# Optimization experiments

Hardware: AMD Instinct MI355X
Metric: run time of the kernel (lower is better)

Reference implementation:

```python
import jax, jax.numpy as jnp
import numpy as np

B, D, DP, H = 65536, 512, 256, 8
HD = D // H  # head dim = 64
EPS = 1e-5


def _layernorm(x, gamma, beta):
    mu = jnp.mean(x, axis=-1, keepdims=True)
    var = jnp.var(x, axis=-1, keepdims=True)
    return (x - mu) * jax.lax.rsqrt(var + EPS) * gamma + beta


def setup_inputs() -> dict:
    key = jax.random.key(0)
    ks = jax.random.split(key, 16)
    n = lambda k, shape, s=0.02: (jax.random.normal(k, shape, jnp.float32) * s)
    return {
        "cell_emb": jax.random.normal(ks[0], (B, D), jnp.float32),
        "pert_emb": jax.random.normal(ks[1], (B, DP), jnp.float32),
        # perturbation_proj: Linear(DP -> D)
        "Wp": n(ks[2], (D, DP)), "bp": jnp.zeros((D,), jnp.float32),
        # MultiheadAttention in/out projections (each D x D)
        "Wq": n(ks[3], (D, D)), "bq": jnp.zeros((D,), jnp.float32),
        "Wk": n(ks[4], (D, D)), "bk": jnp.zeros((D,), jnp.float32),
        "Wv": n(ks[5], (D, D)), "bv": jnp.zeros((D,), jnp.float32),
        "Wo": n(ks[6], (D, D)), "bo": jnp.zeros((D,), jnp.float32),
        # norm1, norm2
        "g1": jnp.ones((D,), jnp.float32), "be1": jnp.zeros((D,), jnp.float32),
        "g2": jnp.ones((D,), jnp.float32), "be2": jnp.zeros((D,), jnp.float32),
        # FFN: Linear(D -> 2D), GELU, Linear(2D -> D)
        "W1": n(ks[7], (2 * D, D)), "b1": jnp.zeros((2 * D,), jnp.float32),
        "W2": n(ks[8], (D, 2 * D)), "b2": jnp.zeros((D,), jnp.float32),
    }


def reference(cell_emb, pert_emb, Wp, bp, Wq, bq, Wk, bk, Wv, bv, Wo, bo,
              g1, be1, g2, be2, W1, b1, W2, b2):
    # kv = perturbation_proj(pert_emb), length-1 KV sequence
    kv = pert_emb @ Wp.T + bp                       # (B, D)
    # MultiheadAttention with q_len = kv_len = 1
    q = (cell_emb @ Wq.T + bq).reshape(B, H, HD)    # (B, H, HD)
    k = (kv @ Wk.T + bk).reshape(B, H, HD)
    v = (kv @ Wv.T + bv).reshape(B, H, HD)
    # scores over a single key -> softmax yields 1, kept for faithfulness
    logits = jnp.sum(q * k, axis=-1, keepdims=True) / jnp.sqrt(jnp.float32(HD))  # (B, H, 1)
    w = jax.nn.softmax(logits, axis=-1)             # == ones (single key)
    attn = (w * v).reshape(B, D)
    attn_out = attn @ Wo.T + bo                     # (B, D)
    x = _layernorm(cell_emb + attn_out, g1, be1)
    # FFN with exact (erf) GELU, matching torch nn.GELU default
    h = jax.nn.gelu(x @ W1.T + b1, approximate=False)
    ffn_out = h @ W2.T + b2
    return _layernorm(x + ffn_out, g2, be2)
```

## Files before the change

kernel.cpp:

```cpp
#include <hip/hip_runtime.h>
#include <hip/hip_bf16.h>

typedef __bf16 bf16_t;
typedef __attribute__((ext_vector_type(8))) __bf16 bf16x8;
typedef __attribute__((ext_vector_type(4))) float f32x4;

__global__ void prep_wvp(const float* __restrict__ Wv, const float* __restrict__ Wp,
                         const float* __restrict__ bp, const float* __restrict__ bv,
                         float* __restrict__ Wvp, float* __restrict__ bvp) {
  const int i = blockIdx.x;
  const int j = threadIdx.x;
  float a = 0.f;
  for (int d = 0; d < 512; ++d) a += Wv[i * 512 + d] * Wp[d * 256 + j];
  Wvp[i * 256 + j] = a;
  if (j == 0) {
    float b = 0.f;
    for (int d = 0; d < 512; ++d) b += Wv[i * 512 + d] * bp[d];
    bvp[i] = b + bv[i];
  }
}

__global__ void prep_wc(const float* __restrict__ Wo, const float* __restrict__ bo,
                        const float* __restrict__ Wvp, const float* __restrict__ bvp,
                        bf16_t* __restrict__ Wc, float* __restrict__ bcomb) {
  const int o = blockIdx.x;
  const int j = threadIdx.x;
  float a = 0.f;
  for (int i = 0; i < 512; ++i) a += Wo[o * 512 + i] * Wvp[i * 256 + j];
  const int g = o >> 4, rr = o & 15, t = j >> 5, q = (j >> 3) & 3, e = j & 7;
  Wc[((((size_t)g * 8 + t) * 64) + q * 16 + rr) * 8 + e] = (bf16_t)a;
  if (j == 0) {
    float b = 0.f;
    for (int i = 0; i < 512; ++i) b += Wo[o * 512 + i] * bvp[i];
    bcomb[o] = b + bo[o];
  }
}

__global__ void prep_cast(const float* __restrict__ W1, const float* __restrict__ W2,
                          bf16_t* __restrict__ W1b, bf16_t* __restrict__ W2b) {
  const int idx = (blockIdx.x * 256 + threadIdx.x) * 8;
  const float* s;
  bf16_t* d;
  if (idx < 524288) {
    const int o = idx >> 9, k = idx & 511;
    const int g = o >> 4, rr = o & 15, t = k >> 5, q = (k >> 3) & 3;
    s = W1 + idx;
    d = W1b + ((((size_t)g * 16 + t) * 64) + q * 16 + rr) * 8;
  } else {
    const int i2 = idx - 524288;
    const int o = i2 >> 10, k = i2 & 1023;
    const int g = o >> 4, rr = o & 15, t = k >> 5, q = (k >> 3) & 3;
    s = W2 + i2;
    d = W2b + ((((size_t)g * 32 + t) * 64) + q * 16 + rr) * 8;
  }
  float4 u0 = *(const float4*)s;
  float4 u1 = *(const float4*)(s + 4);
  bf16x8 v;
  v[0] = (bf16_t)u0.x; v[1] = (bf16_t)u0.y; v[2] = (bf16_t)u0.z; v[3] = (bf16_t)u0.w;
  v[4] = (bf16_t)u1.x; v[5] = (bf16_t)u1.y; v[6] = (bf16_t)u1.z; v[7] = (bf16_t)u1.w;
  *(bf16x8*)d = v;
}


__device__ __forceinline__ int alay(int row, int k) {
  const int rr = row & 15;
  const int c = (k >> 3) & 3;
  return (((k >> 5) & 15) * 4 + (row >> 4)) * 512 +
         (rr * 4 + (c ^ ((rr >> 1) & 3))) * 8 + (k & 7);
}

template <int STEPS>
__device__ __forceinline__ void kloop8(const bf16_t* __restrict__ lA_,
                                       const bf16_t* __restrict__ Bp,
                                       int g0, int SB, int soff,
                                       int fRd, int awin, int lane,
                                       f32x4 (&acc)[2][8]) {
  auto bfrag = [&](int j, int s) {
    return *(const bf16x8*)(Bp + ((size_t)((g0 + j) * SB + (soff + s)) * 64 + lane) * 8);
  };
  bf16x8 bA[4], bB[4];
#pragma unroll
  for (int j = 0; j < 4; ++j) bA[j] = bfrag(j, 0);
#pragma unroll 2
  for (int s = 0; s < STEPS; ++s) {
#pragma unroll
    for (int j = 0; j < 4; ++j) bB[j] = bfrag(4 + j, s);
    bf16x8 af[2];
#pragma unroll
    for (int i = 0; i < 2; ++i)
      af[i] = *(const bf16x8*)&lA_[(s * 4 + awin + i) * 512 + fRd];
    __builtin_amdgcn_s_setprio(1);
#pragma unroll
    for (int j = 0; j < 4; ++j)
#pragma unroll
      for (int i = 0; i < 2; ++i)
        acc[i][j] = __builtin_amdgcn_mfma_f32_16x16x32_bf16(af[i], bA[j], acc[i][j], 0, 0, 0);
    __builtin_amdgcn_s_setprio(0);
    if (s + 1 < STEPS) {
#pragma unroll
      for (int j = 0; j < 4; ++j) bA[j] = bfrag(j, s + 1);
    }
    __builtin_amdgcn_s_setprio(1);
#pragma unroll
    for (int j = 0; j < 4; ++j)
#pragma unroll
      for (int i = 0; i < 2; ++i)
        acc[i][4 + j] = __builtin_amdgcn_mfma_f32_16x16x32_bf16(af[i], bB[j], acc[i][4 + j], 0, 0, 0);
    __builtin_amdgcn_s_setprio(0);
  }
}

__global__ __launch_bounds__(512, 1) void fused_block(
    const float* __restrict__ pert, const bf16_t* __restrict__ Wc,
    const float* __restrict__ bcomb, const float* __restrict__ cell,
    const float* __restrict__ g1, const float* __restrict__ be1,
    const bf16_t* __restrict__ W1b, const float* __restrict__ b1,
    const bf16_t* __restrict__ W2b, const float* __restrict__ b2,
    const float* __restrict__ g2, const float* __restrict__ be2,
    float* __restrict__ out) {

  __shared__ __align__(16) bf16_t lX[64 * 512];
  __shared__ __align__(16) bf16_t lH[64 * 512];
  __shared__ float rs[4][64];
  __shared__ float rss[4][64];

  const int t = threadIdx.x;
  const int m0 = blockIdx.x * 64;
  const int lane = t & 63;
  const int w = t >> 6;
  const int wr = w >> 2;
  const int wc = w & 3;
  const int r = lane & 15;
  const int q = lane >> 4;
  const int qs = q ^ ((r >> 1) & 3);
  const int fRd = r * 32 + qs * 8;
  const int awin = 2 * wr;

#pragma unroll
  for (int u = 0; u < 4; ++u) {
    const int g = u * 512 + t;
    const int row = g >> 5;
    const int c = g & 31;
    const float* src = pert + (size_t)(m0 + row) * 256 + c * 8;
    float4 u0 = *(const float4*)src;
    float4 u1 = *(const float4*)(src + 4);
    bf16x8 v;
    v[0] = (bf16_t)u0.x; v[1] = (bf16_t)u0.y; v[2] = (bf16_t)u0.z; v[3] = (bf16_t)u0.w;
    v[4] = (bf16_t)u1.x; v[5] = (bf16_t)u1.y; v[6] = (bf16_t)u1.z; v[7] = (bf16_t)u1.w;
    *(bf16x8*)&lH[alay(row, c * 8)] = v;
  }
  __syncthreads();

  f32x4 acc1[2][8];
#pragma unroll
  for (int i = 0; i < 2; ++i)
#pragma unroll
    for (int j = 0; j < 8; ++j)
#pragma unroll
      for (int p = 0; p < 4; ++p) acc1[i][j][p] = 0.f;

  kloop8<8>(lH, Wc, 8 * wc, 8, 0, fRd, awin, lane, acc1);

  {
    float s_[2][4], ss_[2][4];
#pragma unroll
    for (int i = 0; i < 2; ++i)
#pragma unroll
      for (int p = 0; p < 4; ++p) { s_[i][p] = 0.f; ss_[i][p] = 0.f; }
    float bb[8];
#pragma unroll
    for (int j = 0; j < 8; ++j) bb[j] = bcomb[128 * wc + 16 * j + r];
#pragma unroll
    for (int i = 0; i < 2; ++i)
#pragma unroll
      for (int p = 0; p < 4; ++p) {
        const int rowl = 32 * wr + 16 * i + 4 * q + p;
#pragma unroll
        for (int j = 0; j < 8; ++j) {
          const int col = 128 * wc + 16 * j + r;
          float v = acc1[i][j][p] + bb[j] + cell[(size_t)(m0 + rowl) * 512 + col];
          acc1[i][j][p] = v;
          s_[i][p] += v;
          ss_[i][p] += v * v;
        }
      }
#pragma unroll
    for (int m = 1; m <= 8; m <<= 1)
#pragma unroll
      for (int i = 0; i < 2; ++i)
#pragma unroll
        for (int p = 0; p < 4; ++p) {
          s_[i][p] += __shfl_xor(s_[i][p], m);
          ss_[i][p] += __shfl_xor(ss_[i][p], m);
        }
    if (r == 0) {
#pragma unroll
      for (int i = 0; i < 2; ++i)
#pragma unroll
        for (int p = 0; p < 4; ++p) {
          const int rowl = 32 * wr + 16 * i + 4 * q + p;
          rs[wc][rowl] = s_[i][p];
          rss[wc][rowl] = ss_[i][p];
        }
    }
    __syncthreads();
    float mu[2][4], inv[2][4];
#pragma unroll
    for (int i = 0; i < 2; ++i)
#pragma unroll
      for (int p = 0; p < 4; ++p) {
        const int rowl = 32 * wr + 16 * i + 4 * q + p;
        float tS = rs[0][rowl] + rs[1][rowl] + rs[2][rowl] + rs[3][rowl];
        float tQ = rss[0][rowl] + rss[1][rowl] + rss[2][rowl] + rss[3][rowl];
        float m_ = tS * (1.0f / 512.0f);
        float v_ = tQ * (1.0f / 512.0f) - m_ * m_;
        mu[i][p] = m_;
        inv[i][p] = rsqrtf(v_ + 1e-5f);
      }
    float ga[8], be[8];
#pragma unroll
    for (int j = 0; j < 8; ++j) {
      ga[j] = g1[128 * wc + 16 * j + r];
      be[j] = be1[128 * wc + 16 * j + r];
    }
#pragma unroll
    for (int i = 0; i < 2; ++i)
#pragma unroll
      for (int p = 0; p < 4; ++p) {
        const int rowl = 32 * wr + 16 * i + 4 * q + p;
#pragma unroll
        for (int j = 0; j < 8; ++j) {
          const int col = 128 * wc + 16 * j + r;
          float v = (acc1[i][j][p] - mu[i][p]) * inv[i][p] * ga[j] + be[j];
          lX[alay(rowl, col)] = (bf16_t)v;
        }
      }
  }
  __syncthreads();

  f32x4 acc3[2][8];
#pragma unroll
  for (int i = 0; i < 2; ++i)
#pragma unroll
    for (int j = 0; j < 8; ++j)
#pragma unroll
      for (int p = 0; p < 4; ++p) acc3[i][j][p] = 0.f;

  for (int hh = 0; hh < 2; ++hh) {
#pragma unroll
    for (int i = 0; i < 2; ++i)
#pragma unroll
      for (int j = 0; j < 8; ++j)
#pragma unroll
        for (int p = 0; p < 4; ++p) acc1[i][j][p] = 0.f;
    kloop8<16>(lX, W1b, 32 * hh + 8 * wc, 16, 0, fRd, awin, lane, acc1);
    {
      float bb1[8];
#pragma unroll
      for (int j = 0; j < 8; ++j) bb1[j] = b1[512 * hh + 128 * wc + 16 * j + r];
#pragma unroll
      for (int i = 0; i < 2; ++i)
#pragma unroll
        for (int p = 0; p < 4; ++p) {
          const int rowl = 32 * wr + 16 * i + 4 * q + p;
#pragma unroll
          for (int j = 0; j < 8; ++j) {
            const int col = 128 * wc + 16 * j + r;
            float v = acc1[i][j][p] + bb1[j];
            float g = 0.5f * v * (1.0f + erff(v * 0.70710678118654752f));
            lH[alay(rowl, col)] = (bf16_t)g;
          }
        }
    }
    __syncthreads();
    kloop8<16>(lH, W2b, 8 * wc, 32, 16 * hh, fRd, awin, lane, acc3);
    if (hh == 0) __syncthreads();
  }

  {
    float s_[2][4], ss_[2][4];
#pragma unroll
    for (int i = 0; i < 2; ++i)
#pragma unroll
      for (int p = 0; p < 4; ++p) { s_[i][p] = 0.f; ss_[i][p] = 0.f; }
    float bb2[8];
#pragma unroll
    for (int j = 0; j < 8; ++j) bb2[j] = b2[128 * wc + 16 * j + r];
#pragma unroll
    for (int i = 0; i < 2; ++i)
#pragma unroll
      for (int p = 0; p < 4; ++p) {
        const int rowl = 32 * wr + 16 * i + 4 * q + p;
#pragma unroll
        for (int j = 0; j < 8; ++j) {
          const int col = 128 * wc + 16 * j + r;
          float v = acc3[i][j][p] + bb2[j] + (float)lX[alay(rowl, col)];
          acc3[i][j][p] = v;
          s_[i][p] += v;
          ss_[i][p] += v * v;
        }
      }
#pragma unroll
    for (int m = 1; m <= 8; m <<= 1)
#pragma unroll
      for (int i = 0; i < 2; ++i)
#pragma unroll
        for (int p = 0; p < 4; ++p) {
          s_[i][p] += __shfl_xor(s_[i][p], m);
          ss_[i][p] += __shfl_xor(ss_[i][p], m);
        }
    __syncthreads();
    if (r == 0) {
#pragma unroll
      for (int i = 0; i < 2; ++i)
#pragma unroll
        for (int p = 0; p < 4; ++p) {
          const int rowl = 32 * wr + 16 * i + 4 * q + p;
          rs[wc][rowl] = s_[i][p];
          rss[wc][rowl] = ss_[i][p];
        }
    }
    __syncthreads();
    float mu[2][4], inv[2][4];
#pragma unroll
    for (int i = 0; i < 2; ++i)
#pragma unroll
      for (int p = 0; p < 4; ++p) {
        const int rowl = 32 * wr + 16 * i + 4 * q + p;
        float tS = rs[0][rowl] + rs[1][rowl] + rs[2][rowl] + rs[3][rowl];
        float tQ = rss[0][rowl] + rss[1][rowl] + rss[2][rowl] + rss[3][rowl];
        float m_ = tS * (1.0f / 512.0f);
        float v_ = tQ * (1.0f / 512.0f) - m_ * m_;
        mu[i][p] = m_;
        inv[i][p] = rsqrtf(v_ + 1e-5f);
      }
    float ga[8], be[8];
#pragma unroll
    for (int j = 0; j < 8; ++j) {
      ga[j] = g2[128 * wc + 16 * j + r];
      be[j] = be2[128 * wc + 16 * j + r];
    }
#pragma unroll
    for (int i = 0; i < 2; ++i)
#pragma unroll
      for (int p = 0; p < 4; ++p) {
        const int rowl = 32 * wr + 16 * i + 4 * q + p;
#pragma unroll
        for (int j = 0; j < 8; ++j) {
          const int col = 128 * wc + 16 * j + r;
          out[(size_t)(m0 + rowl) * 512 + col] =
              (acc3[i][j][p] - mu[i][p]) * inv[i][p] * ga[j] + be[j];
        }
      }
  }
}

extern "C" void kernel_launch(void* const* d_in, const int* in_sizes, int n_in,
                              void* d_out, int out_size, void* d_ws, size_t ws_size,
                              hipStream_t stream) {
  const float* cell = (const float*)d_in[0];
  const float* pert = (const float*)d_in[1];
  const float* Wp   = (const float*)d_in[2];
  const float* bp   = (const float*)d_in[3];
  const float* Wv   = (const float*)d_in[8];
  const float* bv   = (const float*)d_in[9];
  const float* Wo   = (const float*)d_in[10];
  const float* bo   = (const float*)d_in[11];
  const float* g1   = (const float*)d_in[12];
  const float* be1  = (const float*)d_in[13];
  const float* g2   = (const float*)d_in[14];
  const float* be2  = (const float*)d_in[15];
  const float* W1   = (const float*)d_in[16];
  const float* b1   = (const float*)d_in[17];
  const float* W2   = (const float*)d_in[18];
  const float* b2   = (const float*)d_in[19];

  char* ws = (char*)d_ws;
  float*  Wvp   = (float*)(ws + 0);
  float*  bvp   = (float*)(ws + 524288);
  float*  bcomb = (float*)(ws + 526336);
  bf16_t* Wc    = (bf16_t*)(ws + 528384);
  bf16_t* W1b   = (bf16_t*)(ws + 790528);
  bf16_t* W2b   = (bf16_t*)(ws + 1839104);
  (void)in_sizes; (void)n_in; (void)out_size; (void)ws_size;

  prep_wvp<<<512, 256, 0, stream>>>(Wv, Wp, bp, bv, Wvp, bvp);
  prep_wc<<<512, 256, 0, stream>>>(Wo, bo, Wvp, bvp, Wc, bcomb);
  prep_cast<<<512, 256, 0, stream>>>(W1, W2, W1b, W2b);

  fused_block<<<1024, 512, 0, stream>>>(pert, Wc, bcomb, cell, g1, be1,
                                        W1b, b1, W2b, b2, g2, be2,
                                        (float*)d_out);
}
```

Baseline: 651.9 us.

## Split FFN hidden dimension into four quarter chunks to shrink LDS and registers

The FFN hidden dimension is now processed in four 256-wide chunks instead of two 512-wide halves. The GELU intermediate buffer in LDS is halved and the per-chunk accumulator drops to 2x4 tiles, reducing register and shared-memory pressure. The kloop helper is generalized to take a template N-tile count. In exchange there are more barriers and more, shorter K-loops, with less B-fragment reuse per A load in the W1 stage.

```diff
diff --git a/kernel.cpp b/kernel.cpp
--- a/kernel.cpp
+++ b/kernel.cpp
@@ -69,43 +69,44 @@
          (rr * 4 + (c ^ ((rr >> 1) & 3))) * 8 + (k & 7);
 }
 
-template <int STEPS>
-__device__ __forceinline__ void kloop8(const bf16_t* __restrict__ lA_,
-                                       const bf16_t* __restrict__ Bp,
-                                       int g0, int SB, int soff,
-                                       int fRd, int awin, int lane,
-                                       f32x4 (&acc)[2][8]) {
+template <int STEPS, int NJ>
+__device__ __forceinline__ void kloop(const bf16_t* __restrict__ lA_,
+                                      const bf16_t* __restrict__ Bp,
+                                      int g0, int SB, int soff,
+                                      int fRd, int awin, int lane,
+                                      f32x4 (&acc)[2][NJ]) {
+  constexpr int H = NJ / 2;
   auto bfrag = [&](int j, int s) {
     return *(const bf16x8*)(Bp + ((size_t)((g0 + j) * SB + (soff + s)) * 64 + lane) * 8);
   };
-  bf16x8 bA[4], bB[4];
-#pragma unroll
-  for (int j = 0; j < 4; ++j) bA[j] = bfrag(j, 0);
+  bf16x8 bA[H], bB[H];
+#pragma unroll
+  for (int j = 0; j < H; ++j) bA[j] = bfrag(j, 0);
 #pragma unroll 2
   for (int s = 0; s < STEPS; ++s) {
 #pragma unroll
-    for (int j = 0; j < 4; ++j) bB[j] = bfrag(4 + j, s);
+    for (int j = 0; j < H; ++j) bB[j] = bfrag(H + j, s);
     bf16x8 af[2];
 #pragma unroll
     for (int i = 0; i < 2; ++i)
       af[i] = *(const bf16x8*)&lA_[(s * 4 + awin + i) * 512 + fRd];
     __builtin_amdgcn_s_setprio(1);
 #pragma unroll
-    for (int j = 0; j < 4; ++j)
+    for (int j = 0; j < H; ++j)
 #pragma unroll
       for (int i = 0; i < 2; ++i)
         acc[i][j] = __builtin_amdgcn_mfma_f32_16x16x32_bf16(af[i], bA[j], acc[i][j], 0, 0, 0);
     __builtin_amdgcn_s_setprio(0);
     if (s + 1 < STEPS) {
 #pragma unroll
-      for (int j = 0; j < 4; ++j) bA[j] = bfrag(j, s + 1);
+      for (int j = 0; j < H; ++j) bA[j] = bfrag(j, s + 1);
     }
     __builtin_amdgcn_s_setprio(1);
 #pragma unroll
-    for (int j = 0; j < 4; ++j)
-#pragma unroll
-      for (int i = 0; i < 2; ++i)
-        acc[i][4 + j] = __builtin_amdgcn_mfma_f32_16x16x32_bf16(af[i], bB[j], acc[i][4 + j], 0, 0, 0);
+    for (int j = 0; j < H; ++j)
+#pragma unroll
+      for (int i = 0; i < 2; ++i)
+        acc[i][H + j] = __builtin_amdgcn_mfma_f32_16x16x32_bf16(af[i], bB[j], acc[i][H + j], 0, 0, 0);
     __builtin_amdgcn_s_setprio(0);
   }
 }
@@ -120,7 +121,7 @@
     float* __restrict__ out) {
 
   __shared__ __align__(16) bf16_t lX[64 * 512];
-  __shared__ __align__(16) bf16_t lH[64 * 512];
+  __shared__ __align__(16) bf16_t lH[64 * 256];
   __shared__ float rs[4][64];
   __shared__ float rss[4][64];
 
@@ -151,17 +152,16 @@
   }
   __syncthreads();
 
-  f32x4 acc1[2][8];
-#pragma unroll
-  for (int i = 0; i < 2; ++i)
-#pragma unroll
-    for (int j = 0; j < 8; ++j)
-#pragma unroll
-      for (int p = 0; p < 4; ++p) acc1[i][j][p] = 0.f;
-
-  kloop8<8>(lH, Wc, 8 * wc, 8, 0, fRd, awin, lane, acc1);
-
   {
+    f32x4 acc1[2][8];
+#pragma unroll
+    for (int i = 0; i < 2; ++i)
+#pragma unroll
+      for (int j = 0; j < 8; ++j)
+#pragma unroll
+        for (int p = 0; p < 4; ++p) acc1[i][j][p] = 0.f;
+    kloop<8, 8>(lH, Wc, 8 * wc, 8, 0, fRd, awin, lane, acc1);
+
     float s_[2][4], ss_[2][4];
 #pragma unroll
     for (int i = 0; i < 2; ++i)
@@ -246,35 +246,36 @@
 #pragma unroll
       for (int p = 0; p < 4; ++p) acc3[i][j][p] = 0.f;
 
-  for (int hh = 0; hh < 2; ++hh) {
-#pragma unroll
-    for (int i = 0; i < 2; ++i)
-#pragma unroll
-      for (int j = 0; j < 8; ++j)
-#pragma unroll
-        for (int p = 0; p < 4; ++p) acc1[i][j][p] = 0.f;
-    kloop8<16>(lX, W1b, 32 * hh + 8 * wc, 16, 0, fRd, awin, lane, acc1);
+  for (int qh = 0; qh < 4; ++qh) {
     {
-      float bb1[8];
-#pragma unroll
-      for (int j = 0; j < 8; ++j) bb1[j] = b1[512 * hh + 128 * wc + 16 * j + r];
+      f32x4 accq[2][4];
+#pragma unroll
+      for (int i = 0; i < 2; ++i)
+#pragma unroll
+        for (int j = 0; j < 4; ++j)
+#pragma unroll
+          for (int p = 0; p < 4; ++p) accq[i][j][p] = 0.f;
+      kloop<16, 4>(lX, W1b, 16 * qh + 4 * wc, 16, 0, fRd, awin, lane, accq);
+      float bb1[4];
+#pragma unroll
+      for (int j = 0; j < 4; ++j) bb1[j] = b1[256 * qh + 64 * wc + 16 * j + r];
 #pragma unroll
       for (int i = 0; i < 2; ++i)
 #pragma unroll
         for (int p = 0; p < 4; ++p) {
           const int rowl = 32 * wr + 16 * i + 4 * q + p;
 #pragma unroll
-          for (int j = 0; j < 8; ++j) {
-            const int col = 128 * wc + 16 * j + r;
-            float v = acc1[i][j][p] + bb1[j];
+          for (int j = 0; j < 4; ++j) {
+            const int col = 64 * wc + 16 * j + r;
+            float v = accq[i][j][p] + bb1[j];
             float g = 0.5f * v * (1.0f + erff(v * 0.70710678118654752f));
             lH[alay(rowl, col)] = (bf16_t)g;
           }
         }
     }
     __syncthreads();
-    kloop8<16>(lH, W2b, 8 * wc, 32, 16 * hh, fRd, awin, lane, acc3);
-    if (hh == 0) __syncthreads();
+    kloop<8, 8>(lH, W2b, 8 * wc, 32, 8 * qh, fRd, awin, lane, acc3);
+    __syncthreads();
   }
 
   {
```

Result: faster. 628.7 us (-3.6%).
